# Kernel tuning notes

Measured on AMD Instinct MI355X. Metric: run time of the kernel, lower is better.

Reference implementation:

```python
import jax, jax.numpy as jnp
import numpy as np

N, E, G, H, V, L = 100000, 1000000, 1000, 128, 64, 4
NEG_SLOPE = 0.2

def lrelu(x):
    return jnp.where(x >= 0, x, NEG_SLOPE * x)

def setup_inputs() -> dict:
    key = jax.random.key(0)
    ks = jax.random.split(key, 24)
    s = 0.05
    inp = {
        'nfeats': jax.random.randint(ks[0], (N, 9), 0, V, dtype=jnp.int32),
        'efeats': jax.random.randint(ks[1], (E, 3), 0, 4, dtype=jnp.int32),
        'src': jax.random.randint(ks[2], (E,), 0, N, dtype=jnp.int32),
        'dst': jax.random.randint(ks[3], (E,), 0, N, dtype=jnp.int32),
        'graph_ids': jnp.sort(jax.random.randint(ks[4], (N,), 0, G, dtype=jnp.int32)),
        'atom_emb': jax.random.normal(ks[5], (9, V, H), jnp.float32) * s,
        'Wq': jax.random.normal(ks[6], (L, H, H), jnp.float32) * s,
        'bq': jnp.zeros((L, H), jnp.float32),
        'Wk': jax.random.normal(ks[7], (L, H, H), jnp.float32) * s,
        'bk': jnp.zeros((L, H), jnp.float32),
        'Wr': jax.random.normal(ks[8], (L, H, H), jnp.float32) * s,
        'br': jnp.zeros((L, H), jnp.float32),
        'W1': jax.random.normal(ks[9], (H, H // 2), jnp.float32) * s,
        'b1': jnp.zeros((H // 2,), jnp.float32),
        'g1': jnp.ones((H // 2,), jnp.float32),
        'beta1': jnp.zeros((H // 2,), jnp.float32),
        'W2': jax.random.normal(ks[10], (H // 2, H // 4), jnp.float32) * s,
        'b2': jnp.zeros((H // 4,), jnp.float32),
        'g2': jnp.ones((H // 4,), jnp.float32),
        'beta2': jnp.zeros((H // 4,), jnp.float32),
        'W3': jax.random.normal(ks[11], (H // 4, 1), jnp.float32) * s,
        'b3': jnp.zeros((1,), jnp.float32),
    }
    return inp

def batchnorm(x, g, b):
    mu = jnp.mean(x, axis=0)
    var = jnp.var(x, axis=0)
    return (x - mu) * jax.lax.rsqrt(var + 1e-5) * g + b

def reference(nfeats, efeats, src, dst, graph_ids, atom_emb, Wq, bq, Wk, bk, Wr, br,
              W1, b1, g1, beta1, W2, b2, g2, beta2, W3, b3):
    # AtomEncoder: sum of per-feature embeddings -> [N, H]
    h = jnp.sum(atom_emb[jnp.arange(9)[None, :], nfeats], axis=1)
    for l in range(L):
        q = h @ Wq[l] + bq[l]            # dst-side transform [N,H]
        k = h @ Wk[l] + bk[l]            # src-side transform [N,H]
        m = lrelu(q[dst] + k[src])       # per-edge message [E,H]
        agg = jax.ops.segment_sum(m, dst, num_segments=N)  # [N,H]
        h = lrelu(agg @ Wr[l] + br[l])   # norm='none' -> identity, then activation
    hg = jax.ops.segment_sum(h, graph_ids, num_segments=G)  # sum pooling [G,H]
    x = lrelu(batchnorm(hg @ W1 + b1, g1, beta1))
    x = lrelu(batchnorm(x @ W2 + b2, g2, beta2))
    return x @ W3 + b3
```

## Files before the change

kernel.cpp:

```cpp
#include <hip/hip_runtime.h>

#define NN 100000
#define NP 100096
#define NE 1000000
#define NG 1000
#define H 128
#define NLAYER 4
#define NEG 0.2f
#define SCAN_BLOCKS 98

using short8 = __attribute__((ext_vector_type(8))) short;
using fx4 = __attribute__((ext_vector_type(4))) float;

__device__ __forceinline__ float lrelu(float x) { return x >= 0.f ? x : NEG * x; }

__device__ __forceinline__ unsigned short f2bf(float f) {
    union { float f; unsigned int u; } v;
    v.f = f;
    return (unsigned short)((v.u + 0x7fffu + ((v.u >> 16) & 1u)) >> 16);
}
__device__ __forceinline__ float bf2f(unsigned short h) {
    union { unsigned int u; float f; } v;
    v.u = ((unsigned int)h) << 16;
    return v.f;
}
__device__ __forceinline__ float bflo(unsigned int u) {
    union { unsigned int x; float f; } v;
    v.x = u << 16;
    return v.f;
}
__device__ __forceinline__ float bfhi(unsigned int u) {
    union { unsigned int x; float f; } v;
    v.x = u & 0xffff0000u;
    return v.f;
}

__global__ __launch_bounds__(256) void k_atom(const int* __restrict__ nfeats,
                                              const float* __restrict__ emb,
                                              unsigned short* __restrict__ h) {
    int node = blockIdx.x * 4 + (threadIdx.x >> 6);
    if (node >= NN) return;
    int lane = threadIdx.x & 63;
    int c = lane * 2;
    float ax = 0.f, ay = 0.f;
#pragma unroll
    for (int f = 0; f < 9; ++f) {
        int idx = nfeats[node * 9 + f];
        float2 e = *(const float2*)(emb + (size_t)((f << 6) + idx) * H + c);
        ax += e.x;
        ay += e.y;
    }
    unsigned int packed = (unsigned int)f2bf(ax) | ((unsigned int)f2bf(ay) << 16);
    *(unsigned int*)(h + (size_t)node * H + c) = packed;
}

__global__ __launch_bounds__(256) void k_wt(const float* __restrict__ Wq,
                                            const float* __restrict__ Wk,
                                            const float* __restrict__ Wr,
                                            unsigned short* __restrict__ WT) {
    int mat = blockIdx.x;
    int l = mat / 3;
    int kind = mat - l * 3;
    const float* src = (kind == 0 ? Wq : kind == 1 ? Wk : Wr) + (size_t)l * H * H;
    unsigned short* dst = WT + (size_t)mat * H * H;
    for (int idx = threadIdx.x; idx < H * H; idx += 256) {
        int kk = idx >> 7, n = idx & 127;
        dst[n * H + kk] = f2bf(src[idx]);
    }
}

__global__ __launch_bounds__(256) void k_hist(const int* __restrict__ dst, int* __restrict__ deg) {
    int i = blockIdx.x * blockDim.x + threadIdx.x;
    if (i * 4 >= NE) return;
    int4 d = *(const int4*)(dst + i * 4);
    atomicAdd(&deg[d.x], 1);
    atomicAdd(&deg[d.y], 1);
    atomicAdd(&deg[d.z], 1);
    atomicAdd(&deg[d.w], 1);
}

__global__ __launch_bounds__(1024) void k_scan1(const int* __restrict__ deg,
                                                int* __restrict__ rowp,
                                                int* __restrict__ bsum) {
    __shared__ int tmp[1024];
    int t = threadIdx.x;
    int i = blockIdx.x * 1024 + t;
    int v = (i < NN) ? deg[i] : 0;
    tmp[t] = v;
    __syncthreads();
    for (int off = 1; off < 1024; off <<= 1) {
        int u = (t >= off) ? tmp[t - off] : 0;
        __syncthreads();
        tmp[t] += u;
        __syncthreads();
    }
    if (i < NN) rowp[i] = tmp[t] - v;
    if (t == 1023) bsum[blockIdx.x] = tmp[1023];
}

__global__ __launch_bounds__(128) void k_scan2(int* __restrict__ bsum) {
    __shared__ int tmp[128];
    int t = threadIdx.x;
    int v = (t < SCAN_BLOCKS) ? bsum[t] : 0;
    tmp[t] = v;
    __syncthreads();
    for (int off = 1; off < 128; off <<= 1) {
        int u = (t >= off) ? tmp[t - off] : 0;
        __syncthreads();
        tmp[t] += u;
        __syncthreads();
    }
    if (t < SCAN_BLOCKS) bsum[t] = tmp[t] - v;
}

#define SCAN3_BLOCKS ((NN + 255) / 256)
__global__ __launch_bounds__(256) void k_scan3g(const int* __restrict__ bsum,
                                                int* __restrict__ rowp,
                                                int* __restrict__ cursor,
                                                const int* __restrict__ gid,
                                                int* __restrict__ gstart) {
    int bid = blockIdx.x;
    int t = threadIdx.x;
    if (bid < SCAN3_BLOCKS) {
        int i = bid * 256 + t;
        if (i < NN) {
            int v = rowp[i] + bsum[i >> 10];
            rowp[i] = v;
            cursor[i] = v;
        }
        if (i == 0) rowp[NN] = NE;
    } else {
        int g = (bid - SCAN3_BLOCKS) * 256 + t;
        if (g > NG) return;
        if (g == NG) { gstart[NG] = NN; return; }
        int lo = 0, hi = NN;
        while (lo < hi) {
            int mid = (lo + hi) >> 1;
            if (gid[mid] < g) lo = mid + 1; else hi = mid;
        }
        gstart[g] = lo;
    }
}

__global__ __launch_bounds__(256) void k_scatter(const int* __restrict__ src,
                                                 const int* __restrict__ dst,
                                                 int* __restrict__ cursor,
                                                 int* __restrict__ csr_src) {
    int i = blockIdx.x * blockDim.x + threadIdx.x;
    if (i * 4 >= NE) return;
    int4 s = *(const int4*)(src + i * 4);
    int4 d = *(const int4*)(dst + i * 4);
    csr_src[atomicAdd(&cursor[d.x], 1)] = s.x;
    csr_src[atomicAdd(&cursor[d.y], 1)] = s.y;
    csr_src[atomicAdd(&cursor[d.z], 1)] = s.z;
    csr_src[atomicAdd(&cursor[d.w], 1)] = s.w;
}

__global__ __launch_bounds__(256) void k_qk_mfma(const unsigned short* __restrict__ h,
                                                 const unsigned short* __restrict__ WTq,
                                                 const float* __restrict__ bq,
                                                 const unsigned short* __restrict__ WTk,
                                                 const float* __restrict__ bk,
                                                 unsigned short* __restrict__ q,
                                                 unsigned short* __restrict__ k) {
    int lane = threadIdx.x & 63;
    int wave = threadIdx.x >> 6;
    int row0 = blockIdx.x * 128 + wave * 32;
    int lrow = lane & 15;
    int lk = (lane >> 4) << 3;

    short8 a[2][4];
#pragma unroll
    for (int rt = 0; rt < 2; ++rt)
#pragma unroll
        for (int ks = 0; ks < 4; ++ks)
            a[rt][ks] = *(const short8*)(h + (size_t)(row0 + rt * 16 + lrow) * H + ks * 32 + lk);

    fx4 aq[2][8], ak[2][8];
#pragma unroll
    for (int ct = 0; ct < 8; ++ct) {
        float vq = bq[ct * 16 + lrow];
        float vk = bk[ct * 16 + lrow];
#pragma unroll
        for (int rt = 0; rt < 2; ++rt) {
            aq[rt][ct] = fx4{vq, vq, vq, vq};
            ak[rt][ct] = fx4{vk, vk, vk, vk};
        }
    }

#pragma unroll
    for (int ks = 0; ks < 4; ++ks)
#pragma unroll
        for (int ct = 0; ct < 8; ++ct) {
            short8 wq = *(const short8*)(WTq + (ct * 16 + lrow) * H + ks * 32 + lk);
            short8 wk = *(const short8*)(WTk + (ct * 16 + lrow) * H + ks * 32 + lk);
#pragma unroll
            for (int rt = 0; rt < 2; ++rt) {
                aq[rt][ct] = __builtin_amdgcn_mfma_f32_16x16x32_bf16(a[rt][ks], wq, aq[rt][ct], 0, 0, 0);
                ak[rt][ct] = __builtin_amdgcn_mfma_f32_16x16x32_bf16(a[rt][ks], wk, ak[rt][ct], 0, 0, 0);
            }
        }

#pragma unroll
    for (int rt = 0; rt < 2; ++rt)
#pragma unroll
        for (int ct = 0; ct < 8; ++ct)
#pragma unroll
            for (int rg = 0; rg < 4; ++rg) {
                int r = row0 + rt * 16 + ((lane >> 4) << 2) + rg;
                if (r < NN) {
                    q[(size_t)r * H + ct * 16 + lrow] = f2bf(aq[rt][ct][rg]);
                    k[(size_t)r * H + ct * 16 + lrow] = f2bf(ak[rt][ct][rg]);
                }
            }
}

__global__ __launch_bounds__(256) void k_r_mfma(const unsigned short* __restrict__ agg,
                                                const unsigned short* __restrict__ WTr,
                                                const float* __restrict__ br,
                                                unsigned short* __restrict__ hout) {
    int lane = threadIdx.x & 63;
    int wave = threadIdx.x >> 6;
    int row0 = blockIdx.x * 128 + wave * 32;
    int lrow = lane & 15;
    int lk = (lane >> 4) << 3;

    short8 a[2][4];
#pragma unroll
    for (int rt = 0; rt < 2; ++rt)
#pragma unroll
        for (int ks = 0; ks < 4; ++ks)
            a[rt][ks] = *(const short8*)(agg + (size_t)(row0 + rt * 16 + lrow) * H + ks * 32 + lk);

    fx4 acc[2][8];
#pragma unroll
    for (int ct = 0; ct < 8; ++ct) {
        float v = br[ct * 16 + lrow];
#pragma unroll
        for (int rt = 0; rt < 2; ++rt) acc[rt][ct] = fx4{v, v, v, v};
    }

#pragma unroll
    for (int ks = 0; ks < 4; ++ks)
#pragma unroll
        for (int ct = 0; ct < 8; ++ct) {
            short8 w = *(const short8*)(WTr + (ct * 16 + lrow) * H + ks * 32 + lk);
#pragma unroll
            for (int rt = 0; rt < 2; ++rt)
                acc[rt][ct] = __builtin_amdgcn_mfma_f32_16x16x32_bf16(a[rt][ks], w, acc[rt][ct], 0, 0, 0);
        }

#pragma unroll
    for (int rt = 0; rt < 2; ++rt)
#pragma unroll
        for (int ct = 0; ct < 8; ++ct)
#pragma unroll
            for (int rg = 0; rg < 4; ++rg) {
                int r = row0 + rt * 16 + ((lane >> 4) << 2) + rg;
                if (r < NN)
                    hout[(size_t)r * H + ct * 16 + lrow] = f2bf(lrelu(acc[rt][ct][rg]));
            }
}

__global__ __launch_bounds__(256) void k_rqk_mfma(const unsigned short* __restrict__ agg,
                                                  const unsigned short* __restrict__ WTr,
                                                  const float* __restrict__ br,
                                                  const unsigned short* __restrict__ WTq,
                                                  const float* __restrict__ bq,
                                                  const unsigned short* __restrict__ WTk,
                                                  const float* __restrict__ bk,
                                                  unsigned short* __restrict__ q,
                                                  unsigned short* __restrict__ k) {
    __shared__ unsigned short hls[4][32][136];
    int lane = threadIdx.x & 63;
    int wave = threadIdx.x >> 6;
    int row0 = blockIdx.x * 128 + wave * 32;
    int lrow = lane & 15;
    int lk = (lane >> 4) << 3;

    short8 a[2][4];
#pragma unroll
    for (int rt = 0; rt < 2; ++rt)
#pragma unroll
        for (int ks = 0; ks < 4; ++ks)
            a[rt][ks] = *(const short8*)(agg + (size_t)(row0 + rt * 16 + lrow) * H + ks * 32 + lk);

    fx4 acc[2][8];
#pragma unroll
    for (int ct = 0; ct < 8; ++ct) {
        float v = br[ct * 16 + lrow];
#pragma unroll
        for (int rt = 0; rt < 2; ++rt) acc[rt][ct] = fx4{v, v, v, v};
    }

#pragma unroll
    for (int ks = 0; ks < 4; ++ks)
#pragma unroll
        for (int ct = 0; ct < 8; ++ct) {
            short8 w = *(const short8*)(WTr + (ct * 16 + lrow) * H + ks * 32 + lk);
#pragma unroll
            for (int rt = 0; rt < 2; ++rt)
                acc[rt][ct] = __builtin_amdgcn_mfma_f32_16x16x32_bf16(a[rt][ks], w, acc[rt][ct], 0, 0, 0);
        }

#pragma unroll
    for (int rt = 0; rt < 2; ++rt)
#pragma unroll
        for (int ct = 0; ct < 8; ++ct)
#pragma unroll
            for (int rg = 0; rg < 4; ++rg) {
                int lr = rt * 16 + ((lane >> 4) << 2) + rg;
                hls[wave][lr][ct * 16 + lrow] = f2bf(lrelu(acc[rt][ct][rg]));
            }

    short8 a2[2][4];
#pragma unroll
    for (int rt = 0; rt < 2; ++rt)
#pragma unroll
        for (int ks = 0; ks < 4; ++ks)
            a2[rt][ks] = *(const short8*)&hls[wave][rt * 16 + lrow][ks * 32 + lk];

    fx4 aq[2][8], ak[2][8];
#pragma unroll
    for (int ct = 0; ct < 8; ++ct) {
        float vq = bq[ct * 16 + lrow];
        float vk = bk[ct * 16 + lrow];
#pragma unroll
        for (int rt = 0; rt < 2; ++rt) {
            aq[rt][ct] = fx4{vq, vq, vq, vq};
            ak[rt][ct] = fx4{vk, vk, vk, vk};
        }
    }

#pragma unroll
    for (int ks = 0; ks < 4; ++ks)
#pragma unroll
        for (int ct = 0; ct < 8; ++ct) {
            short8 wq = *(const short8*)(WTq + (ct * 16 + lrow) * H + ks * 32 + lk);
            short8 wk = *(const short8*)(WTk + (ct * 16 + lrow) * H + ks * 32 + lk);
#pragma unroll
            for (int rt = 0; rt < 2; ++rt) {
                aq[rt][ct] = __builtin_amdgcn_mfma_f32_16x16x32_bf16(a2[rt][ks], wq, aq[rt][ct], 0, 0, 0);
                ak[rt][ct] = __builtin_amdgcn_mfma_f32_16x16x32_bf16(a2[rt][ks], wk, ak[rt][ct], 0, 0, 0);
            }
        }

#pragma unroll
    for (int rt = 0; rt < 2; ++rt)
#pragma unroll
        for (int ct = 0; ct < 8; ++ct)
#pragma unroll
            for (int rg = 0; rg < 4; ++rg) {
                int r = row0 + rt * 16 + ((lane >> 4) << 2) + rg;
                if (r < NN) {
                    q[(size_t)r * H + ct * 16 + lrow] = f2bf(aq[rt][ct][rg]);
                    k[(size_t)r * H + ct * 16 + lrow] = f2bf(ak[rt][ct][rg]);
                }
            }
}

__global__ __launch_bounds__(256) void k_agg(const unsigned short* __restrict__ q,
                                             const unsigned short* __restrict__ kk,
                                             const int* __restrict__ rowp,
                                             const int* __restrict__ csr_src,
                                             unsigned short* __restrict__ agg) {
    int node = blockIdx.x * 4 + (threadIdx.x >> 6);
    if (node >= NN) return;
    int lane = threadIdx.x & 63;
    int qt = lane >> 4;
    int ql = lane & 15;
    int start = rowp[node];
    int end = rowp[node + 1];

    uint4 qp = *(const uint4*)(q + (size_t)node * H + ql * 8);
    float qv0 = bflo(qp.x), qv1 = bfhi(qp.x), qv2 = bflo(qp.y), qv3 = bfhi(qp.y);
    float qv4 = bflo(qp.z), qv5 = bfhi(qp.z), qv6 = bflo(qp.w), qv7 = bfhi(qp.w);
    float a0 = 0.f, a1 = 0.f, a2 = 0.f, a3 = 0.f, a4 = 0.f, a5 = 0.f, a6 = 0.f, a7 = 0.f;

    for (int base = start; base < end; base += 64) {
        int cnt = end - base;
        if (cnt > 64) cnt = 64;
        int sid = (lane < cnt) ? csr_src[base + lane] : 0;
        int cnt8 = (cnt + 7) & ~7;
        for (int j = 0; j < cnt8; j += 8) {
            int jj0 = j + qt;
            int jj1 = j + 4 + qt;
            int s0 = __shfl(sid, jj0);
            int s1 = __shfl(sid, jj1);
            uint4 kp0 = *(const uint4*)(kk + (size_t)s0 * H + ql * 8);
            uint4 kp1 = *(const uint4*)(kk + (size_t)s1 * H + ql * 8);
            if (jj0 < cnt) {
                a0 += lrelu(qv0 + bflo(kp0.x));
                a1 += lrelu(qv1 + bfhi(kp0.x));
                a2 += lrelu(qv2 + bflo(kp0.y));
                a3 += lrelu(qv3 + bfhi(kp0.y));
                a4 += lrelu(qv4 + bflo(kp0.z));
                a5 += lrelu(qv5 + bfhi(kp0.z));
                a6 += lrelu(qv6 + bflo(kp0.w));
                a7 += lrelu(qv7 + bfhi(kp0.w));
            }
            if (jj1 < cnt) {
                a0 += lrelu(qv0 + bflo(kp1.x));
                a1 += lrelu(qv1 + bfhi(kp1.x));
                a2 += lrelu(qv2 + bflo(kp1.y));
                a3 += lrelu(qv3 + bfhi(kp1.y));
                a4 += lrelu(qv4 + bflo(kp1.z));
                a5 += lrelu(qv5 + bfhi(kp1.z));
                a6 += lrelu(qv6 + bflo(kp1.w));
                a7 += lrelu(qv7 + bfhi(kp1.w));
            }
        }
    }
    a0 += __shfl_xor(a0, 16); a0 += __shfl_xor(a0, 32);
    a1 += __shfl_xor(a1, 16); a1 += __shfl_xor(a1, 32);
    a2 += __shfl_xor(a2, 16); a2 += __shfl_xor(a2, 32);
    a3 += __shfl_xor(a3, 16); a3 += __shfl_xor(a3, 32);
    a4 += __shfl_xor(a4, 16); a4 += __shfl_xor(a4, 32);
    a5 += __shfl_xor(a5, 16); a5 += __shfl_xor(a5, 32);
    a6 += __shfl_xor(a6, 16); a6 += __shfl_xor(a6, 32);
    a7 += __shfl_xor(a7, 16); a7 += __shfl_xor(a7, 32);
    if (qt == 0) {
        uint4 o;
        o.x = (unsigned int)f2bf(a0) | ((unsigned int)f2bf(a1) << 16);
        o.y = (unsigned int)f2bf(a2) | ((unsigned int)f2bf(a3) << 16);
        o.z = (unsigned int)f2bf(a4) | ((unsigned int)f2bf(a5) << 16);
        o.w = (unsigned int)f2bf(a6) | ((unsigned int)f2bf(a7) << 16);
        *(uint4*)(agg + (size_t)node * H + ql * 8) = o;
    }
}

__global__ __launch_bounds__(256) void k_pool_seg(const unsigned short* __restrict__ h,
                                                  const int* __restrict__ gstart,
                                                  float* __restrict__ hg) {
    int g = blockIdx.x * 4 + (threadIdx.x >> 6);
    if (g >= NG) return;
    int lane = threadIdx.x & 63;
    int s = gstart[g], e = gstart[g + 1];
    float ax = 0.f, ay = 0.f;
    for (int n = s; n < e; ++n) {
        unsigned int hp = *(const unsigned int*)(h + (size_t)n * H + lane * 2);
        ax += bflo(hp);
        ay += bfhi(hp);
    }
    float2 o;
    o.x = ax;
    o.y = ay;
    *(float2*)(hg + (size_t)g * H + lane * 2) = o;
}

__global__ __launch_bounds__(256) void k_mlp1(const float* __restrict__ hg,
                                              const float* __restrict__ W1,
                                              const float* __restrict__ b1,
                                              float* __restrict__ x1) {
    __shared__ float W1s[128 * 64];
    __shared__ float hgs[4 * 128];
    int t = threadIdx.x;
    int g0 = blockIdx.x * 4;
#pragma unroll
    for (int i = 0; i < 32; ++i) W1s[t + i * 256] = W1[t + i * 256];
    for (int i = t; i < 4 * 128; i += 256) hgs[i] = hg[(size_t)g0 * H + i];
    __syncthreads();
    int g = t >> 6, c = t & 63;
    float acc = b1[c];
    const float* row = hgs + g * 128;
    for (int j = 0; j < 128; ++j) acc += row[j] * W1s[j * 64 + c];
    x1[(g0 + g) * 64 + c] = acc;
}

template <int C>
__global__ __launch_bounds__(1024) void k_bnstats(const float* __restrict__ x,
                                                  float* __restrict__ stats) {
    __shared__ float red[1024];
    __shared__ float mus[C];
    int t = threadIdx.x;
    int c = t & (C - 1), rc = t / C;
    const int R = 1024 / C;
    float s = 0.f;
    for (int g = rc; g < NG; g += R) s += x[g * C + c];
    red[t] = s;
    __syncthreads();
    if (t < C) {
        float S = 0.f;
        for (int i = 0; i < R; ++i) S += red[i * C + t];
        float mu = S / NG;
        mus[t] = mu;
        stats[t] = mu;
    }
    __syncthreads();
    float mu = mus[c];
    float s2 = 0.f;
    for (int g = rc; g < NG; g += R) {
        float d = x[g * C + c] - mu;
        s2 += d * d;
    }
    red[t] = s2;
    __syncthreads();
    if (t < C) {
        float Q = 0.f;
        for (int i = 0; i < R; ++i) Q += red[i * C + t];
        stats[C + t] = rsqrtf(Q / NG + 1e-5f);
    }
}

__global__ __launch_bounds__(256) void k_mlp2f(const float* __restrict__ x1,
                                               const float* __restrict__ st,
                                               const float* __restrict__ g1,
                                               const float* __restrict__ be1,
                                               const float* __restrict__ W2,
                                               const float* __restrict__ b2,
                                               float* __restrict__ x2) {
    __shared__ float W2s[64 * 32];
    __shared__ float x1s[8 * 64];
    int t = threadIdx.x;
    int g0 = blockIdx.x * 8;
#pragma unroll
    for (int i = 0; i < 8; ++i) W2s[t + i * 256] = W2[t + i * 256];
#pragma unroll
    for (int i = 0; i < 2; ++i) {
        int idx = t + i * 256;
        int c = idx & 63;
        float v = x1[(size_t)g0 * 64 + idx];
        v = (v - st[c]) * st[64 + c] * g1[c] + be1[c];
        x1s[idx] = lrelu(v);
    }
    __syncthreads();
    int g = t >> 5, c = t & 31;
    float acc = b2[c];
    const float* row = x1s + g * 64;
    for (int j = 0; j < 64; ++j) acc += row[j] * W2s[j * 32 + c];
    x2[(g0 + g) * 32 + c] = acc;
}

__global__ __launch_bounds__(256) void k_mlp3f(const float* __restrict__ x2,
                                               const float* __restrict__ st,
                                               const float* __restrict__ g2,
                                               const float* __restrict__ be2,
                                               const float* __restrict__ W3,
                                               const float* __restrict__ b3,
                                               float* __restrict__ out) {
    int g = blockIdx.x * blockDim.x + threadIdx.x;
    if (g >= NG) return;
    float acc = b3[0];
    for (int j = 0; j < 32; ++j) {
        float v = (x2[g * 32 + j] - st[j]) * st[32 + j] * g2[j] + be2[j];
        acc += lrelu(v) * W3[j];
    }
    out[g] = acc;
}

extern "C" void kernel_launch(void* const* d_in, const int* in_sizes, int n_in,
                              void* d_out, int out_size, void* d_ws, size_t ws_size,
                              hipStream_t stream) {
    const int* nfeats = (const int*)d_in[0];
    const int* src = (const int*)d_in[2];
    const int* dst = (const int*)d_in[3];
    const int* gid = (const int*)d_in[4];
    const float* emb = (const float*)d_in[5];
    const float* Wq = (const float*)d_in[6];
    const float* bq = (const float*)d_in[7];
    const float* Wk = (const float*)d_in[8];
    const float* bk = (const float*)d_in[9];
    const float* Wr = (const float*)d_in[10];
    const float* br = (const float*)d_in[11];
    const float* W1 = (const float*)d_in[12];
    const float* b1 = (const float*)d_in[13];
    const float* g1 = (const float*)d_in[14];
    const float* be1 = (const float*)d_in[15];
    const float* W2 = (const float*)d_in[16];
    const float* b2 = (const float*)d_in[17];
    const float* g2 = (const float*)d_in[18];
    const float* be2 = (const float*)d_in[19];
    const float* W3 = (const float*)d_in[20];
    const float* b3 = (const float*)d_in[21];
    float* out = (float*)d_out;

    size_t nh = (size_t)NP * H;
    unsigned short* P0 = (unsigned short*)d_ws;
    unsigned short* P1 = P0 + nh;
    unsigned short* P2 = P1 + nh;
    unsigned short* WT = P2 + nh;
    float* hg = (float*)(WT + 12 * H * H);
    float* x1 = hg + (size_t)NG * H;
    float* x2 = x1 + (size_t)NG * 64;
    float* st = x2 + (size_t)NG * 32;
    int* cursor = (int*)(st + 2 * 64);
    int* rowp = cursor + NN;
    int* bsum = rowp + NN + 1;
    int* csr_src = bsum + 128;
    int* gstart = csr_src + NE;

    hipMemsetAsync(cursor, 0, NN * sizeof(int), stream);
    k_hist<<<(NE / 4 + 255) / 256, 256, 0, stream>>>(dst, cursor);
    k_scan1<<<SCAN_BLOCKS, 1024, 0, stream>>>(cursor, rowp, bsum);
    k_scan2<<<1, 128, 0, stream>>>(bsum);
    k_scan3g<<<SCAN3_BLOCKS + 4, 256, 0, stream>>>(bsum, rowp, cursor, gid, gstart);
    k_scatter<<<(NE / 4 + 255) / 256, 256, 0, stream>>>(src, dst, cursor, csr_src);

    k_wt<<<12, 256, 0, stream>>>(Wq, Wk, Wr, WT);
    k_atom<<<NN / 4, 256, 0, stream>>>(nfeats, emb, P0);

    const int NB = NP / 128;
    k_qk_mfma<<<NB, 256, 0, stream>>>(P0, WT + 0 * H * H, bq, WT + 1 * H * H, bk, P1, P2);
    for (int l = 0; l < NLAYER; ++l) {
        k_agg<<<(NN + 3) / 4, 256, 0, stream>>>(P1, P2, rowp, csr_src, P0);
        if (l < NLAYER - 1) {
            k_rqk_mfma<<<NB, 256, 0, stream>>>(P0, WT + (size_t)(l * 3 + 2) * H * H, br + l * H,
                                               WT + (size_t)((l + 1) * 3 + 0) * H * H, bq + (l + 1) * H,
                                               WT + (size_t)((l + 1) * 3 + 1) * H * H, bk + (l + 1) * H,
                                               P1, P2);
        } else {
            k_r_mfma<<<NB, 256, 0, stream>>>(P0, WT + (size_t)(l * 3 + 2) * H * H, br + l * H, P1);
        }
    }

    k_pool_seg<<<(NG + 3) / 4, 256, 0, stream>>>(P1, gstart, hg);

    k_mlp1<<<NG / 4, 256, 0, stream>>>(hg, W1, b1, x1);
    k_bnstats<64><<<1, 1024, 0, stream>>>(x1, st);
    k_mlp2f<<<NG / 8, 256, 0, stream>>>(x1, st, g1, be1, W2, b2, x2);
    k_bnstats<32><<<1, 1024, 0, stream>>>(x2, st);
    k_mlp3f<<<(NG + 255) / 256, 256, 0, stream>>>(x2, st, g2, be2, W3, b3, out);
}
```

Before: 734.7 us.

## Fuse atom encoder into first QK GEMM, split accumulators, deepen agg gather

Removes the separate atom-embedding kernel and computes the embedding sums directly into MFMA A-fragments inside the first Q/K projection kernel, avoiding a write and reread of the node feature matrix. All MFMA kernels now accumulate over half the output columns per pass, which shrinks the live accumulator registers and is meant to raise occupancy. The aggregation loop issues four neighbor key loads per iteration instead of two to increase memory-level parallelism. The costs are a redundant emb load per row fragment in the fused kernel, extra reloads of the weight tiles across passes, and more wasted lanes on padded neighbor counts.

```diff
diff --git a/kernel.cpp b/kernel.cpp
--- a/kernel.cpp
+++ b/kernel.cpp
@@ -19,11 +19,6 @@
     v.f = f;
     return (unsigned short)((v.u + 0x7fffu + ((v.u >> 16) & 1u)) >> 16);
 }
-__device__ __forceinline__ float bf2f(unsigned short h) {
-    union { unsigned int u; float f; } v;
-    v.u = ((unsigned int)h) << 16;
-    return v.f;
-}
 __device__ __forceinline__ float bflo(unsigned int u) {
     union { unsigned int x; float f; } v;
     v.x = u << 16;
@@ -33,25 +28,6 @@
     union { unsigned int x; float f; } v;
     v.x = u & 0xffff0000u;
     return v.f;
-}
-
-__global__ __launch_bounds__(256) void k_atom(const int* __restrict__ nfeats,
-                                              const float* __restrict__ emb,
-                                              unsigned short* __restrict__ h) {
-    int node = blockIdx.x * 4 + (threadIdx.x >> 6);
-    if (node >= NN) return;
-    int lane = threadIdx.x & 63;
-    int c = lane * 2;
-    float ax = 0.f, ay = 0.f;
-#pragma unroll
-    for (int f = 0; f < 9; ++f) {
-        int idx = nfeats[node * 9 + f];
-        float2 e = *(const float2*)(emb + (size_t)((f << 6) + idx) * H + c);
-        ax += e.x;
-        ay += e.y;
-    }
-    unsigned int packed = (unsigned int)f2bf(ax) | ((unsigned int)f2bf(ay) << 16);
-    *(unsigned int*)(h + (size_t)node * H + c) = packed;
 }
 
 __global__ __launch_bounds__(256) void k_wt(const float* __restrict__ Wq,
@@ -156,13 +132,14 @@
     csr_src[atomicAdd(&cursor[d.w], 1)] = s.w;
 }
 
-__global__ __launch_bounds__(256) void k_qk_mfma(const unsigned short* __restrict__ h,
-                                                 const unsigned short* __restrict__ WTq,
-                                                 const float* __restrict__ bq,
-                                                 const unsigned short* __restrict__ WTk,
-                                                 const float* __restrict__ bk,
-                                                 unsigned short* __restrict__ q,
-                                                 unsigned short* __restrict__ k) {
+__global__ __launch_bounds__(256) void k_aqk_mfma(const int* __restrict__ nfeats,
+                                                  const float* __restrict__ emb,
+                                                  const unsigned short* __restrict__ WTq,
+                                                  const float* __restrict__ bq,
+                                                  const unsigned short* __restrict__ WTk,
+                                                  const float* __restrict__ bk,
+                                                  unsigned short* __restrict__ q,
+                                                  unsigned short* __restrict__ k) {
     int lane = threadIdx.x & 63;
     int wave = threadIdx.x >> 6;
     int row0 = blockIdx.x * 128 + wave * 32;
@@ -171,48 +148,65 @@
 
     short8 a[2][4];
 #pragma unroll
-    for (int rt = 0; rt < 2; ++rt)
+    for (int rt = 0; rt < 2; ++rt) {
+        int row = row0 + rt * 16 + lrow;
+        int crow = row < NN ? row : NN - 1;
+        int fidx[9];
+#pragma unroll
+        for (int f = 0; f < 9; ++f) fidx[f] = nfeats[crow * 9 + f];
+#pragma unroll
+        for (int ks = 0; ks < 4; ++ks) {
+            float s0 = 0.f, s1 = 0.f, s2 = 0.f, s3 = 0.f, s4 = 0.f, s5 = 0.f, s6 = 0.f, s7 = 0.f;
+#pragma unroll
+            for (int f = 0; f < 9; ++f) {
+                const float* e = emb + (size_t)((f << 6) + fidx[f]) * H + ks * 32 + lk;
+                float4 e0 = *(const float4*)e;
+                float4 e1 = *(const float4*)(e + 4);
+                s0 += e0.x; s1 += e0.y; s2 += e0.z; s3 += e0.w;
+                s4 += e1.x; s5 += e1.y; s6 += e1.z; s7 += e1.w;
+            }
+            short8 v;
+            v[0] = (short)f2bf(s0); v[1] = (short)f2bf(s1);
+            v[2] = (short)f2bf(s2); v[3] = (short)f2bf(s3);
+            v[4] = (short)f2bf(s4); v[5] = (short)f2bf(s5);
+            v[6] = (short)f2bf(s6); v[7] = (short)f2bf(s7);
+            a[rt][ks] = v;
+        }
+    }
+
+#pragma unroll
+    for (int pass = 0; pass < 4; ++pass) {
+        const unsigned short* W = (pass < 2) ? WTq : WTk;
+        const float* b = (pass < 2) ? bq : bk;
+        unsigned short* o = (pass < 2) ? q : k;
+        int c0 = (pass & 1) * 4;
+        fx4 acc[2][4];
+#pragma unroll
+        for (int ct = 0; ct < 4; ++ct) {
+            float v = b[(c0 + ct) * 16 + lrow];
+#pragma unroll
+            for (int rt = 0; rt < 2; ++rt) acc[rt][ct] = fx4{v, v, v, v};
+        }
 #pragma unroll
         for (int ks = 0; ks < 4; ++ks)
-            a[rt][ks] = *(const short8*)(h + (size_t)(row0 + rt * 16 + lrow) * H + ks * 32 + lk);
-
-    fx4 aq[2][8], ak[2][8];
-#pragma unroll
-    for (int ct = 0; ct < 8; ++ct) {
-        float vq = bq[ct * 16 + lrow];
-        float vk = bk[ct * 16 + lrow];
-#pragma unroll
-        for (int rt = 0; rt < 2; ++rt) {
-            aq[rt][ct] = fx4{vq, vq, vq, vq};
-            ak[rt][ct] = fx4{vk, vk, vk, vk};
-        }
-    }
-
-#pragma unroll
-    for (int ks = 0; ks < 4; ++ks)
-#pragma unroll
-        for (int ct = 0; ct < 8; ++ct) {
-            short8 wq = *(const short8*)(WTq + (ct * 16 + lrow) * H + ks * 32 + lk);
-            short8 wk = *(const short8*)(WTk + (ct * 16 + lrow) * H + ks * 32 + lk);
-#pragma unroll
-            for (int rt = 0; rt < 2; ++rt) {
-                aq[rt][ct] = __builtin_amdgcn_mfma_f32_16x16x32_bf16(a[rt][ks], wq, aq[rt][ct], 0, 0, 0);
-                ak[rt][ct] = __builtin_amdgcn_mfma_f32_16x16x32_bf16(a[rt][ks], wk, ak[rt][ct], 0, 0, 0);
-            }
-        }
-
-#pragma unroll
-    for (int rt = 0; rt < 2; ++rt)
-#pragma unroll
-        for (int ct = 0; ct < 8; ++ct)
-#pragma unroll
-            for (int rg = 0; rg < 4; ++rg) {
-                int r = row0 + rt * 16 + ((lane >> 4) << 2) + rg;
-                if (r < NN) {
-                    q[(size_t)r * H + ct * 16 + lrow] = f2bf(aq[rt][ct][rg]);
-                    k[(size_t)r * H + ct * 16 + lrow] = f2bf(ak[rt][ct][rg]);
+#pragma unroll
+            for (int ct = 0; ct < 4; ++ct) {
+                short8 w = *(const short8*)(W + ((c0 + ct) * 16 + lrow) * H + ks * 32 + lk);
+#pragma unroll
+                for (int rt = 0; rt < 2; ++rt)
+                    acc[rt][ct] = __builtin_amdgcn_mfma_f32_16x16x32_bf16(a[rt][ks], w, acc[rt][ct], 0, 0, 0);
+            }
+#pragma unroll
+        for (int rt = 0; rt < 2; ++rt)
+#pragma unroll
+            for (int ct = 0; ct < 4; ++ct)
+#pragma unroll
+                for (int rg = 0; rg < 4; ++rg) {
+                    int r = row0 + rt * 16 + ((lane >> 4) << 2) + rg;
+                    if (r < NN)
+                        o[(size_t)r * H + (c0 + ct) * 16 + lrow] = f2bf(acc[rt][ct][rg]);
                 }
-            }
+    }
 }
 
 __global__ __launch_bounds__(256) void k_r_mfma(const unsigned short* __restrict__ agg,
@@ -232,34 +226,36 @@
         for (int ks = 0; ks < 4; ++ks)
             a[rt][ks] = *(const short8*)(agg + (size_t)(row0 + rt * 16 + lrow) * H + ks * 32 + lk);
 
-    fx4 acc[2][8];
-#pragma unroll
-    for (int ct = 0; ct < 8; ++ct) {
-        float v = br[ct * 16 + lrow];
-#pragma unroll
-        for (int rt = 0; rt < 2; ++rt) acc[rt][ct] = fx4{v, v, v, v};
-    }
-
-#pragma unroll
-    for (int ks = 0; ks < 4; ++ks)
-#pragma unroll
-        for (int ct = 0; ct < 8; ++ct) {
-            short8 w = *(const short8*)(WTr + (ct * 16 + lrow) * H + ks * 32 + lk);
-#pragma unroll
-            for (int rt = 0; rt < 2; ++rt)
-                acc[rt][ct] = __builtin_amdgcn_mfma_f32_16x16x32_bf16(a[rt][ks], w, acc[rt][ct], 0, 0, 0);
-        }
-
-#pragma unroll
-    for (int rt = 0; rt < 2; ++rt)
-#pragma unroll
-        for (int ct = 0; ct < 8; ++ct)
-#pragma unroll
-            for (int rg = 0; rg < 4; ++rg) {
-                int r = row0 + rt * 16 + ((lane >> 4) << 2) + rg;
-                if (r < NN)
-                    hout[(size_t)r * H + ct * 16 + lrow] = f2bf(lrelu(acc[rt][ct][rg]));
-            }
+#pragma unroll
+    for (int chf = 0; chf < 2; ++chf) {
+        int c0 = chf * 4;
+        fx4 acc[2][4];
+#pragma unroll
+        for (int ct = 0; ct < 4; ++ct) {
+            float v = br[(c0 + ct) * 16 + lrow];
+#pragma unroll
+            for (int rt = 0; rt < 2; ++rt) acc[rt][ct] = fx4{v, v, v, v};
+        }
+#pragma unroll
+        for (int ks = 0; ks < 4; ++ks)
+#pragma unroll
+            for (int ct = 0; ct < 4; ++ct) {
+                short8 w = *(const short8*)(WTr + ((c0 + ct) * 16 + lrow) * H + ks * 32 + lk);
+#pragma unroll
+                for (int rt = 0; rt < 2; ++rt)
+                    acc[rt][ct] = __builtin_amdgcn_mfma_f32_16x16x32_bf16(a[rt][ks], w, acc[rt][ct], 0, 0, 0);
+            }
+#pragma unroll
+        for (int rt = 0; rt < 2; ++rt)
+#pragma unroll
+            for (int ct = 0; ct < 4; ++ct)
+#pragma unroll
+                for (int rg = 0; rg < 4; ++rg) {
+                    int r = row0 + rt * 16 + ((lane >> 4) << 2) + rg;
+                    if (r < NN)
+                        hout[(size_t)r * H + (c0 + ct) * 16 + lrow] = f2bf(lrelu(acc[rt][ct][rg]));
+                }
+    }
 }
 
 __global__ __launch_bounds__(256) void k_rqk_mfma(const unsigned short* __restrict__ agg,
@@ -285,33 +281,35 @@
         for (int ks = 0; ks < 4; ++ks)
             a[rt][ks] = *(const short8*)(agg + (size_t)(row0 + rt * 16 + lrow) * H + ks * 32 + lk);
 
-    fx4 acc[2][8];
-#pragma unroll
-    for (int ct = 0; ct < 8; ++ct) {
-        float v = br[ct * 16 + lrow];
-#pragma unroll
-        for (int rt = 0; rt < 2; ++rt) acc[rt][ct] = fx4{v, v, v, v};
-    }
-
-#pragma unroll
-    for (int ks = 0; ks < 4; ++ks)
-#pragma unroll
-        for (int ct = 0; ct < 8; ++ct) {
-            short8 w = *(const short8*)(WTr + (ct * 16 + lrow) * H + ks * 32 + lk);
-#pragma unroll
-            for (int rt = 0; rt < 2; ++rt)
-                acc[rt][ct] = __builtin_amdgcn_mfma_f32_16x16x32_bf16(a[rt][ks], w, acc[rt][ct], 0, 0, 0);
-        }
-
-#pragma unroll
-    for (int rt = 0; rt < 2; ++rt)
-#pragma unroll
-        for (int ct = 0; ct < 8; ++ct)
-#pragma unroll
-            for (int rg = 0; rg < 4; ++rg) {
-                int lr = rt * 16 + ((lane >> 4) << 2) + rg;
-                hls[wave][lr][ct * 16 + lrow] = f2bf(lrelu(acc[rt][ct][rg]));
-            }
+#pragma unroll
+    for (int chf = 0; chf < 2; ++chf) {
+        int c0 = chf * 4;
+        fx4 acc[2][4];
+#pragma unroll
+        for (int ct = 0; ct < 4; ++ct) {
+            float v = br[(c0 + ct) * 16 + lrow];
+#pragma unroll
+            for (int rt = 0; rt < 2; ++rt) acc[rt][ct] = fx4{v, v, v, v};
+        }
+#pragma unroll
+        for (int ks = 0; ks < 4; ++ks)
+#pragma unroll
+            for (int ct = 0; ct < 4; ++ct) {
+                short8 w = *(const short8*)(WTr + ((c0 + ct) * 16 + lrow) * H + ks * 32 + lk);
+#pragma unroll
+                for (int rt = 0; rt < 2; ++rt)
+                    acc[rt][ct] = __builtin_amdgcn_mfma_f32_16x16x32_bf16(a[rt][ks], w, acc[rt][ct], 0, 0, 0);
+            }
+#pragma unroll
+        for (int rt = 0; rt < 2; ++rt)
+#pragma unroll
+            for (int ct = 0; ct < 4; ++ct)
+#pragma unroll
+                for (int rg = 0; rg < 4; ++rg) {
+                    int lr = rt * 16 + ((lane >> 4) << 2) + rg;
+                    hls[wave][lr][(c0 + ct) * 16 + lrow] = f2bf(lrelu(acc[rt][ct][rg]));
+                }
+    }
 
     short8 a2[2][4];
 #pragma unroll
@@ -320,43 +318,39 @@
         for (int ks = 0; ks < 4; ++ks)
             a2[rt][ks] = *(const short8*)&hls[wave][rt * 16 + lrow][ks * 32 + lk];
 
-    fx4 aq[2][8], ak[2][8];
-#pragma unroll
-    for (int ct = 0; ct < 8; ++ct) {
-        float vq = bq[ct * 16 + lrow];
-        float vk = bk[ct * 16 + lrow];
-#pragma unroll
-        for (int rt = 0; rt < 2; ++rt) {
-            aq[rt][ct] = fx4{vq, vq, vq, vq};
-            ak[rt][ct] = fx4{vk, vk, vk, vk};
-        }
-    }
-
-#pragma unroll
-    for (int ks = 0; ks < 4; ++ks)
-#pragma unroll
-        for (int ct = 0; ct < 8; ++ct) {
-            short8 wq = *(const short8*)(WTq + (ct * 16 + lrow) * H + ks * 32 + lk);
-            short8 wk = *(const short8*)(WTk + (ct * 16 + lrow) * H + ks * 32 + lk);
-#pragma unroll
-            for (int rt = 0; rt < 2; ++rt) {
-                aq[rt][ct] = __builtin_amdgcn_mfma_f32_16x16x32_bf16(a2[rt][ks], wq, aq[rt][ct], 0, 0, 0);
-                ak[rt][ct] = __builtin_amdgcn_mfma_f32_16x16x32_bf16(a2[rt][ks], wk, ak[rt][ct], 0, 0, 0);
-            }
-        }
-
-#pragma unroll
-    for (int rt = 0; rt < 2; ++rt)
-#pragma unroll
-        for (int ct = 0; ct < 8; ++ct)
-#pragma unroll
-            for (int rg = 0; rg < 4; ++rg) {
-                int r = row0 + rt * 16 + ((lane >> 4) << 2) + rg;
-                if (r < NN) {
-                    q[(size_t)r * H + ct * 16 + lrow] = f2bf(aq[rt][ct][rg]);
-                    k[(size_t)r * H + ct * 16 + lrow] = f2bf(ak[rt][ct][rg]);
+#pragma unroll
+    for (int pass = 0; pass < 4; ++pass) {
+        const unsigned short* W = (pass < 2) ? WTq : WTk;
+        const float* b = (pass < 2) ? bq : bk;
+        unsigned short* o = (pass < 2) ? q : k;
+        int c0 = (pass & 1) * 4;
+        fx4 acc[2][4];
+#pragma unroll
+        for (int ct = 0; ct < 4; ++ct) {
+            float v = b[(c0 + ct) * 16 + lrow];
+#pragma unroll
+            for (int rt = 0; rt < 2; ++rt) acc[rt][ct] = fx4{v, v, v, v};
+        }
+#pragma unroll
+        for (int ks = 0; ks < 4; ++ks)
+#pragma unroll
+            for (int ct = 0; ct < 4; ++ct) {
+                short8 w = *(const short8*)(W + ((c0 + ct) * 16 + lrow) * H + ks * 32 + lk);
+#pragma unroll
+                for (int rt = 0; rt < 2; ++rt)
+                    acc[rt][ct] = __builtin_amdgcn_mfma_f32_16x16x32_bf16(a2[rt][ks], w, acc[rt][ct], 0, 0, 0);
+            }
+#pragma unroll
+        for (int rt = 0; rt < 2; ++rt)
+#pragma unroll
+            for (int ct = 0; ct < 4; ++ct)
+#pragma unroll
+                for (int rg = 0; rg < 4; ++rg) {
+                    int r = row0 + rt * 16 + ((lane >> 4) << 2) + rg;
+                    if (r < NN)
+                        o[(size_t)r * H + (c0 + ct) * 16 + lrow] = f2bf(acc[rt][ct][rg]);
                 }
-            }
+    }
 }
 
 __global__ __launch_bounds__(256) void k_agg(const unsigned short* __restrict__ q,
@@ -381,33 +375,43 @@
         int cnt = end - base;
         if (cnt > 64) cnt = 64;
         int sid = (lane < cnt) ? csr_src[base + lane] : 0;
-        int cnt8 = (cnt + 7) & ~7;
-        for (int j = 0; j < cnt8; j += 8) {
+        int cnt16 = (cnt + 15) & ~15;
+        for (int j = 0; j < cnt16; j += 16) {
             int jj0 = j + qt;
             int jj1 = j + 4 + qt;
+            int jj2 = j + 8 + qt;
+            int jj3 = j + 12 + qt;
             int s0 = __shfl(sid, jj0);
             int s1 = __shfl(sid, jj1);
+            int s2 = __shfl(sid, jj2);
+            int s3 = __shfl(sid, jj3);
             uint4 kp0 = *(const uint4*)(kk + (size_t)s0 * H + ql * 8);
             uint4 kp1 = *(const uint4*)(kk + (size_t)s1 * H + ql * 8);
+            uint4 kp2 = *(const uint4*)(kk + (size_t)s2 * H + ql * 8);
+            uint4 kp3 = *(const uint4*)(kk + (size_t)s3 * H + ql * 8);
             if (jj0 < cnt) {
-                a0 += lrelu(qv0 + bflo(kp0.x));
-                a1 += lrelu(qv1 + bfhi(kp0.x));
-                a2 += lrelu(qv2 + bflo(kp0.y));
-                a3 += lrelu(qv3 + bfhi(kp0.y));
-                a4 += lrelu(qv4 + bflo(kp0.z));
-                a5 += lrelu(qv5 + bfhi(kp0.z));
-                a6 += lrelu(qv6 + bflo(kp0.w));
-                a7 += lrelu(qv7 + bfhi(kp0.w));
+                a0 += lrelu(qv0 + bflo(kp0.x)); a1 += lrelu(qv1 + bfhi(kp0.x));
+                a2 += lrelu(qv2 + bflo(kp0.y)); a3 += lrelu(qv3 + bfhi(kp0.y));
+                a4 += lrelu(qv4 + bflo(kp0.z)); a5 += lrelu(qv5 + bfhi(kp0.z));
+                a6 += lrelu(qv6 + bflo(kp0.w)); a7 += lrelu(qv7 + bfhi(kp0.w));
             }
             if (jj1 < cnt) {
-                a0 += lrelu(qv0 + bflo(kp1.x));
-                a1 += lrelu(qv1 + bfhi(kp1.x));
-                a2 += lrelu(qv2 + bflo(kp1.y));
-                a3 += lrelu(qv3 + bfhi(kp1.y));
-                a4 += lrelu(qv4 + bflo(kp1.z));
-                a5 += lrelu(qv5 + bfhi(kp1.z));
-                a6 += lrelu(qv6 + bflo(kp1.w));
-                a7 += lrelu(qv7 + bfhi(kp1.w));
+                a0 += lrelu(qv0 + bflo(kp1.x)); a1 += lrelu(qv1 + bfhi(kp1.x));
+                a2 += lrelu(qv2 + bflo(kp1.y)); a3 += lrelu(qv3 + bfhi(kp1.y));
+                a4 += lrelu(qv4 + bflo(kp1.z)); a5 += lrelu(qv5 + bfhi(kp1.z));
+                a6 += lrelu(qv6 + bflo(kp1.w)); a7 += lrelu(qv7 + bfhi(kp1.w));
+            }
+            if (jj2 < cnt) {
+                a0 += lrelu(qv0 + bflo(kp2.x)); a1 += lrelu(qv1 + bfhi(kp2.x));
+                a2 += lrelu(qv2 + bflo(kp2.y)); a3 += lrelu(qv3 + bfhi(kp2.y));
+                a4 += lrelu(qv4 + bflo(kp2.z)); a5 += lrelu(qv5 + bfhi(kp2.z));
+                a6 += lrelu(qv6 + bflo(kp2.w)); a7 += lrelu(qv7 + bfhi(kp2.w));
+            }
+            if (jj3 < cnt) {
+                a0 += lrelu(qv0 + bflo(kp3.x)); a1 += lrelu(qv1 + bfhi(kp3.x));
+                a2 += lrelu(qv2 + bflo(kp3.y)); a3 += lrelu(qv3 + bfhi(kp3.y));
+                a4 += lrelu(qv4 + bflo(kp3.z)); a5 += lrelu(qv5 + bfhi(kp3.z));
+                a6 += lrelu(qv6 + bflo(kp3.w)); a7 += lrelu(qv7 + bfhi(kp3.w));
             }
         }
     }
@@ -597,10 +601,9 @@
     k_scatter<<<(NE / 4 + 255) / 256, 256, 0, stream>>>(src, dst, cursor, csr_src);
 
     k_wt<<<12, 256, 0, stream>>>(Wq, Wk, Wr, WT);
-    k_atom<<<NN / 4, 256, 0, stream>>>(nfeats, emb, P0);
 
     const int NB = NP / 128;
-    k_qk_mfma<<<NB, 256, 0, stream>>>(P0, WT + 0 * H * H, bq, WT + 1 * H * H, bk, P1, P2);
+    k_aqk_mfma<<<NB, 256, 0, stream>>>(nfeats, emb, WT + 0 * H * H, bq, WT + 1 * H * H, bk, P1, P2);
     for (int l = 0; l < NLAYER; ++l) {
         k_agg<<<(NN + 3) / 4, 256, 0, stream>>>(P1, P2, rowp, csr_src, P0);
         if (l < NLAYER - 1) {
```

Result: no change. 730.4 us (-0.6%).
